# Kernel optimization log

Hardware: AMD Instinct MI355X
Metric: run time of the kernel (lower is better)

The kernel has to match this reference:

```python
import jax, jax.numpy as jnp
import numpy as np

N_DATA = 8192
M_QUERIES = 8192

def setup_inputs() -> dict:
    key = jax.random.key(0)
    k1, k2 = jax.random.split(key)
    data = jax.random.uniform(k1, (N_DATA, 3), dtype=jnp.float32)
    queries = jax.random.uniform(k2, (M_QUERIES, 3), dtype=jnp.float32)
    return {"data": data, "queries": queries, "radius": 0.1}

def reference(data, queries, radius):
    """Faithful jax version of native_neighbor_search.

    Returns (neighbors_index, neighbors_row_splits).
    Because jax.jit requires static shapes, neighbors_index is padded to the
    maximal size m*n with -1; the number of valid entries is
    neighbors_row_splits[-1]. Valid entries appear in the same row-major
    (query-ordered) order as torch's nonzero().
    """
    n = data.shape[0]
    m = queries.shape[0]
    # pairwise Euclidean distances [m, n] via the ||q||^2 + ||d||^2 - 2 q.d expansion
    q2 = jnp.sum(queries * queries, axis=1, keepdims=True)          # [m,1]
    d2 = jnp.sum(data * data, axis=1, keepdims=True).T              # [1,n]
    dists = jnp.sqrt(jnp.maximum(q2 + d2 - 2.0 * (queries @ data.T), 0.0))
    mask = dists <= radius                                          # [m,n]
    # CSR row splits: exclusive prefix sum of per-query neighbor counts
    counts = jnp.sum(mask.astype(jnp.int32), axis=1)                # [m]
    row_splits = jnp.concatenate(
        [jnp.zeros((1,), jnp.int32), jnp.cumsum(counts)])           # [m+1]
    # flattened nonzero in row-major order -> column index = flat % n
    (flat_idx,) = jnp.nonzero(mask.ravel(), size=m * n, fill_value=-1)
    neighbors_index = jnp.where(flat_idx >= 0, flat_idx % n, -1).astype(jnp.int32)
    return neighbors_index, row_splits
```

## Files before the change

### kernel.cpp

```cpp
#include <hip/hip_runtime.h>
#include <stdint.h>


#define N8 8192
#define C0 2097152

__device__ __forceinline__ float next_up(float x) {
    return __uint_as_float(__float_as_uint(x) + 1u);
}
__device__ __forceinline__ float next_down(float x) {
    return __uint_as_float(__float_as_uint(x) - 1u);
}

__device__ __forceinline__ float sq_threshold(float r) {
    float T = __fmul_rn(r, r);
    while (__fsqrt_rn(T) > r) T = next_down(T);
    while (__fsqrt_rn(next_up(T)) <= r) T = next_up(T);
    return T;
}

__device__ __forceinline__ float pair_metric(float qx, float qy, float qz, float q2,
                                             float dx, float dy, float dz) {
    float d2 = __fadd_rn(__fadd_rn(__fmul_rn(dx, dx), __fmul_rn(dy, dy)),
                         __fmul_rn(dz, dz));
    float dot = __builtin_fmaf(qz, dz, __builtin_fmaf(qy, dy, __fmul_rn(qx, dx)));
    return __fsub_rn(__fadd_rn(q2, d2), __fmul_rn(2.0f, dot));
}

__device__ __forceinline__ float bc_lane(float x, int j) {
    return __int_as_float(__builtin_amdgcn_readlane(__float_as_int(x), j));
}


__global__ __launch_bounds__(256) void count_then_fill(
    const float* __restrict__ data, const float* __restrict__ queries,
    const float* __restrict__ radius_p, int* __restrict__ out_idx,
    unsigned long long* __restrict__ masks, int* __restrict__ counts) {
    int bid = blockIdx.x;
    int lane = threadIdx.x & 63;
    int wv = threadIdx.x >> 6;

    {
        int u = bid * 4 + wv;
        int c = u >> 6;
        int g = u & 63;
        float T = sq_threshold(radius_p[0]);
        int p = c * 64 + lane;
        float dx = data[3 * p + 0], dy = data[3 * p + 1], dz = data[3 * p + 2];
        float d2 = __fadd_rn(__fadd_rn(__fmul_rn(dx, dx), __fmul_rn(dy, dy)),
                             __fmul_rn(dz, dz));
        for (int s = 0; s < 2; ++s) {
            int qbase = g * 128 + s * 64;
            int q = qbase + lane;
            float qx = queries[3 * q + 0], qy = queries[3 * q + 1],
                  qz = queries[3 * q + 2];
            float q2 = __fadd_rn(__fadd_rn(__fmul_rn(qx, qx), __fmul_rn(qy, qy)),
                                 __fmul_rn(qz, qz));
            unsigned long long parked = 0;
#pragma unroll
            for (int j = 0; j < 64; ++j) {
                float Qx = bc_lane(qx, j), Qy = bc_lane(qy, j);
                float Qz = bc_lane(qz, j), Q2 = bc_lane(q2, j);
                float dot = __builtin_fmaf(Qz, dz,
                              __builtin_fmaf(Qy, dy, __fmul_rn(Qx, dx)));
                float uu = __fsub_rn(__fadd_rn(Q2, d2), __fmul_rn(2.0f, dot));
                unsigned long long mk = __ballot(uu <= T);
                if (lane == j) parked = mk;
            }
            masks[(size_t)(qbase + lane) * 128 + c] = parked;
            atomicAdd(&counts[qbase + lane], __popcll(parked));
        }
    }

    int4* out4 = (int4*)out_idx;
    const int4 v = make_int4(-1, -1, -1, -1);
    const size_t n4 = (size_t)N8 * N8 / 4;
    size_t i = (size_t)(C0 / 4) + (size_t)bid * 256 + threadIdx.x;
    const size_t stride = 2048ull * 256ull;
    for (; i < n4; i += stride) out4[i] = v;
}

__global__ __launch_bounds__(1024) void scan_kernel2(const int* __restrict__ counts,
                                                     int* __restrict__ rs, int m) {
    __shared__ int part[1024];
    int t = threadIdx.x;
    int base = t * 8;
    int c[8];
    int s = 0;
    for (int k = 0; k < 8; ++k) {
        int p = base + k;
        c[k] = (p < m) ? counts[p] : 0;
        s += c[k];
    }
    part[t] = s;
    __syncthreads();
    for (int off = 1; off < 1024; off <<= 1) {
        int v = 0;
        if (t >= off) v = part[t - off];
        __syncthreads();
        if (t >= off) part[t] += v;
        __syncthreads();
    }
    int run = (t == 0) ? 0 : part[t - 1];
    for (int k = 0; k < 8; ++k) {
        int p = base + k;
        if (p < m) rs[p] = run;
        run += c[k];
    }
    if (t == 1023) rs[m] = part[1023];
}

__global__ __launch_bounds__(256) void emit_fill_tail(
    const unsigned long long* __restrict__ masks, const int* __restrict__ rs,
    int* __restrict__ out_idx) {
    int wave = threadIdx.x >> 6;
    int lane = threadIdx.x & 63;
    int q = blockIdx.x * 4 + wave;

    unsigned long long lo = masks[(size_t)q * 128 + lane];
    unsigned long long hi = masks[(size_t)q * 128 + 64 + lane];
    int plo = __popcll(lo), phi = __popcll(hi);
    int ilo = plo, ihi = phi;
    for (int off = 1; off < 64; off <<= 1) {
        int a = __shfl_up(ilo, off, 64);
        int b = __shfl_up(ihi, off, 64);
        if (lane >= off) { ilo += a; ihi += b; }
    }
    int total_lo = __shfl(ilo, 63, 64);
    int base = rs[q];
    int pos_lo = base + ilo - plo;
    int pos_hi = base + total_lo + ihi - phi;
    int jb_lo = lane * 64, jb_hi = (64 + lane) * 64;
    while (lo) {
        int b = __builtin_ctzll(lo);
        out_idx[pos_lo++] = jb_lo + b;
        lo &= lo - 1;
    }
    while (hi) {
        int b = __builtin_ctzll(hi);
        out_idx[pos_hi++] = jb_hi + b;
        hi &= hi - 1;
    }

    int L = rs[N8];
    int Lr = (L + 3) & ~3;
    if (blockIdx.x == 0 && (int)threadIdx.x < (Lr - L))
        out_idx[L + threadIdx.x] = -1;
    int4* out4 = (int4*)out_idx;
    const int4 v = make_int4(-1, -1, -1, -1);
    const int c04 = C0 >> 2;
    int i = (Lr >> 2) + blockIdx.x * 256 + threadIdx.x;
    const int stride = 2048 * 256;
    for (; i < c04; i += stride) out4[i] = v;
}


__global__ __launch_bounds__(256) void fill_kernel(int* __restrict__ out, size_t total) {
    size_t n4 = total >> 2;
    int4* out4 = (int4*)out;
    size_t i = (size_t)blockIdx.x * blockDim.x + threadIdx.x;
    size_t stride = (size_t)gridDim.x * blockDim.x;
    const int4 v = make_int4(-1, -1, -1, -1);
    for (; i < n4; i += stride) out4[i] = v;
    if (blockIdx.x == 0 && threadIdx.x == 0) {
        for (size_t k = n4 << 2; k < total; ++k) out[k] = -1;
    }
}

__global__ __launch_bounds__(256) void count_kernel(
    const float* __restrict__ data, const float* __restrict__ queries,
    const float* __restrict__ radius_p, int n, int m, int* __restrict__ counts) {
    int q = (blockIdx.x * blockDim.x + threadIdx.x) >> 6;
    int lane = threadIdx.x & 63;
    if (q >= m) return;
    float r = radius_p[0];
    float T = sq_threshold(r);
    float qx = queries[3 * q + 0], qy = queries[3 * q + 1], qz = queries[3 * q + 2];
    float q2 = __fadd_rn(__fadd_rn(__fmul_rn(qx, qx), __fmul_rn(qy, qy)),
                         __fmul_rn(qz, qz));
    int cnt = 0;
    for (int j = lane; j < n; j += 64) {
        float u = pair_metric(qx, qy, qz, q2, data[3 * j], data[3 * j + 1], data[3 * j + 2]);
        if (u <= T) cnt++;
    }
    for (int off = 32; off > 0; off >>= 1) cnt += __shfl_down(cnt, off, 64);
    if (lane == 0) counts[q] = cnt;
}

__global__ __launch_bounds__(256) void emit_kernel(
    const float* __restrict__ data, const float* __restrict__ queries,
    const float* __restrict__ radius_p, int n, int m,
    const int* __restrict__ row_splits, int* __restrict__ out_idx) {
    int q = (blockIdx.x * blockDim.x + threadIdx.x) >> 6;
    int lane = threadIdx.x & 63;
    if (q >= m) return;
    float r = radius_p[0];
    float T = sq_threshold(r);
    float qx = queries[3 * q + 0], qy = queries[3 * q + 1], qz = queries[3 * q + 2];
    float q2 = __fadd_rn(__fadd_rn(__fmul_rn(qx, qx), __fmul_rn(qy, qy)),
                         __fmul_rn(qz, qz));
    int base = row_splits[q];
    unsigned long long lane_mask_lt = (lane == 0) ? 0ULL : (~0ULL >> (64 - lane));
    for (int j0 = 0; j0 < n; j0 += 64) {
        int j = j0 + lane;
        bool pred = false;
        if (j < n) {
            float u = pair_metric(qx, qy, qz, q2, data[3 * j], data[3 * j + 1], data[3 * j + 2]);
            pred = (u <= T);
        }
        unsigned long long mask = __ballot(pred);
        if (pred) {
            int pos = base + __popcll(mask & lane_mask_lt);
            out_idx[pos] = j;
        }
        base += __popcll(mask);
    }
}


extern "C" void kernel_launch(void* const* d_in, const int* in_sizes, int n_in,
                              void* d_out, int out_size, void* d_ws, size_t ws_size,
                              hipStream_t stream) {
    const float* data = (const float*)d_in[0];
    const float* queries = (const float*)d_in[1];
    const float* radius = (const float*)d_in[2];
    int n = in_sizes[0] / 3;
    int m = in_sizes[1] / 3;
    int* out = (int*)d_out;
    size_t idx_count = (size_t)m * (size_t)n;
    int* row = out + idx_count;

    size_t mask_bytes = (size_t)N8 * 128 * 8;
    size_t need = mask_bytes + N8 * 4;
    bool fast = (n == N8) && (m == N8) && (ws_size >= need);

    if (fast) {
        unsigned long long* masks = (unsigned long long*)d_ws;
        int* counts = (int*)((char*)d_ws + mask_bytes);
        hipMemsetAsync(counts, 0, N8 * sizeof(int), stream);
        count_then_fill<<<2048, 256, 0, stream>>>(data, queries, radius, out,
                                                  masks, counts);
        scan_kernel2<<<1, 1024, 0, stream>>>(counts, row, m);
        emit_fill_tail<<<2048, 256, 0, stream>>>(masks, row, out);
    } else {
        fill_kernel<<<2048, 256, 0, stream>>>(out, idx_count);
        int blocks = (m * 64 + 255) / 256;
        count_kernel<<<blocks, 256, 0, stream>>>(data, queries, radius, n, m, row);
        scan_kernel2<<<1, 1024, 0, stream>>>(row, row, m);
        emit_kernel<<<blocks, 256, 0, stream>>>(data, queries, radius, n, m, row, out);
    }
}
```

Baseline: 77.53 us.

## Fuse prefix scan into emit kernel with redundant per-block scan

```diff
diff --git a/kernel.cpp b/kernel.cpp
--- a/kernel.cpp
+++ b/kernel.cpp
@@ -4,6 +4,8 @@
 
 #define N8 8192
 #define C0 2097152
+#define C04 (C0 / 4)
+#define N4TOT ((size_t)N8 * N8 / 4)
 
 __device__ __forceinline__ float next_up(float x) {
     return __uint_as_float(__float_as_uint(x) + 1u);
@@ -31,127 +33,132 @@
     return __int_as_float(__builtin_amdgcn_readlane(__float_as_int(x), j));
 }
 
+__device__ __forceinline__ void count_unit(
+    int u, const float* __restrict__ data, const float* __restrict__ queries,
+    float T, unsigned long long* __restrict__ masks, int* __restrict__ counts) {
+    int lane = threadIdx.x & 63;
+    int c = u >> 6;
+    int g = u & 63;
+    int p = c * 64 + lane;
+    float dx = data[3 * p + 0], dy = data[3 * p + 1], dz = data[3 * p + 2];
+    float d2 = __fadd_rn(__fadd_rn(__fmul_rn(dx, dx), __fmul_rn(dy, dy)),
+                         __fmul_rn(dz, dz));
+    for (int s = 0; s < 2; ++s) {
+        int qbase = g * 128 + s * 64;
+        int q = qbase + lane;
+        float qx = queries[3 * q + 0], qy = queries[3 * q + 1],
+              qz = queries[3 * q + 2];
+        float q2 = __fadd_rn(__fadd_rn(__fmul_rn(qx, qx), __fmul_rn(qy, qy)),
+                             __fmul_rn(qz, qz));
+        unsigned long long parked = 0;
+#pragma unroll
+        for (int j = 0; j < 64; ++j) {
+            float Qx = bc_lane(qx, j), Qy = bc_lane(qy, j);
+            float Qz = bc_lane(qz, j), Q2 = bc_lane(q2, j);
+            float dot = __builtin_fmaf(Qz, dz,
+                          __builtin_fmaf(Qy, dy, __fmul_rn(Qx, dx)));
+            float uu = __fsub_rn(__fadd_rn(Q2, d2), __fmul_rn(2.0f, dot));
+            unsigned long long mk = __ballot(uu <= T);
+            if (lane == j) parked = mk;
+        }
+        masks[(size_t)(qbase + lane) * 128 + c] = parked;
+        atomicAdd(&counts[qbase + lane], __popcll(parked));
+    }
+}
+
 
 __global__ __launch_bounds__(256) void count_then_fill(
     const float* __restrict__ data, const float* __restrict__ queries,
     const float* __restrict__ radius_p, int* __restrict__ out_idx,
     unsigned long long* __restrict__ masks, int* __restrict__ counts) {
     int bid = blockIdx.x;
-    int lane = threadIdx.x & 63;
     int wv = threadIdx.x >> 6;
-
     {
-        int u = bid * 4 + wv;
-        int c = u >> 6;
-        int g = u & 63;
         float T = sq_threshold(radius_p[0]);
-        int p = c * 64 + lane;
-        float dx = data[3 * p + 0], dy = data[3 * p + 1], dz = data[3 * p + 2];
-        float d2 = __fadd_rn(__fadd_rn(__fmul_rn(dx, dx), __fmul_rn(dy, dy)),
-                             __fmul_rn(dz, dz));
-        for (int s = 0; s < 2; ++s) {
-            int qbase = g * 128 + s * 64;
-            int q = qbase + lane;
-            float qx = queries[3 * q + 0], qy = queries[3 * q + 1],
-                  qz = queries[3 * q + 2];
-            float q2 = __fadd_rn(__fadd_rn(__fmul_rn(qx, qx), __fmul_rn(qy, qy)),
-                                 __fmul_rn(qz, qz));
-            unsigned long long parked = 0;
-#pragma unroll
-            for (int j = 0; j < 64; ++j) {
-                float Qx = bc_lane(qx, j), Qy = bc_lane(qy, j);
-                float Qz = bc_lane(qz, j), Q2 = bc_lane(q2, j);
-                float dot = __builtin_fmaf(Qz, dz,
-                              __builtin_fmaf(Qy, dy, __fmul_rn(Qx, dx)));
-                float uu = __fsub_rn(__fadd_rn(Q2, d2), __fmul_rn(2.0f, dot));
-                unsigned long long mk = __ballot(uu <= T);
-                if (lane == j) parked = mk;
-            }
-            masks[(size_t)(qbase + lane) * 128 + c] = parked;
-            atomicAdd(&counts[qbase + lane], __popcll(parked));
-        }
-    }
-
+        count_unit(bid * 4 + wv, data, queries, T, masks, counts);
+    }
     int4* out4 = (int4*)out_idx;
     const int4 v = make_int4(-1, -1, -1, -1);
-    const size_t n4 = (size_t)N8 * N8 / 4;
-    size_t i = (size_t)(C0 / 4) + (size_t)bid * 256 + threadIdx.x;
+    size_t i = (size_t)C04 + (size_t)bid * 256 + threadIdx.x;
     const size_t stride = 2048ull * 256ull;
-    for (; i < n4; i += stride) out4[i] = v;
-}
-
-__global__ __launch_bounds__(1024) void scan_kernel2(const int* __restrict__ counts,
-                                                     int* __restrict__ rs, int m) {
-    __shared__ int part[1024];
+    for (; i < N4TOT; i += stride) out4[i] = v;
+}
+
+__global__ __launch_bounds__(256) void scanemit_fill_tail(
+    const unsigned long long* __restrict__ masks, const int* __restrict__ counts,
+    int* __restrict__ out_idx, int* __restrict__ rs) {
+    __shared__ int part[256];
+    __shared__ int s_cnt[32];
+    __shared__ int s_base[4];
+    int b = blockIdx.x;
     int t = threadIdx.x;
-    int base = t * 8;
-    int c[8];
+    int wave = t >> 6;
+    int lane = t & 63;
+
     int s = 0;
-    for (int k = 0; k < 8; ++k) {
-        int p = base + k;
-        c[k] = (p < m) ? counts[p] : 0;
-        s += c[k];
-    }
+#pragma unroll 8
+    for (int k = 0; k < 32; ++k) s += counts[t * 32 + k];
     part[t] = s;
     __syncthreads();
-    for (int off = 1; off < 1024; off <<= 1) {
+    for (int off = 1; off < 256; off <<= 1) {
         int v = 0;
         if (t >= off) v = part[t - off];
         __syncthreads();
         if (t >= off) part[t] += v;
         __syncthreads();
     }
-    int run = (t == 0) ? 0 : part[t - 1];
-    for (int k = 0; k < 8; ++k) {
-        int p = base + k;
-        if (p < m) rs[p] = run;
-        run += c[k];
-    }
-    if (t == 1023) rs[m] = part[1023];
-}
-
-__global__ __launch_bounds__(256) void emit_fill_tail(
-    const unsigned long long* __restrict__ masks, const int* __restrict__ rs,
-    int* __restrict__ out_idx) {
-    int wave = threadIdx.x >> 6;
-    int lane = threadIdx.x & 63;
-    int q = blockIdx.x * 4 + wave;
-
-    unsigned long long lo = masks[(size_t)q * 128 + lane];
-    unsigned long long hi = masks[(size_t)q * 128 + 64 + lane];
-    int plo = __popcll(lo), phi = __popcll(hi);
-    int ilo = plo, ihi = phi;
-    for (int off = 1; off < 64; off <<= 1) {
-        int a = __shfl_up(ilo, off, 64);
-        int b = __shfl_up(ihi, off, 64);
-        if (lane >= off) { ilo += a; ihi += b; }
-    }
-    int total_lo = __shfl(ilo, 63, 64);
-    int base = rs[q];
-    int pos_lo = base + ilo - plo;
-    int pos_hi = base + total_lo + ihi - phi;
-    int jb_lo = lane * 64, jb_hi = (64 + lane) * 64;
-    while (lo) {
-        int b = __builtin_ctzll(lo);
-        out_idx[pos_lo++] = jb_lo + b;
-        lo &= lo - 1;
-    }
-    while (hi) {
-        int b = __builtin_ctzll(hi);
-        out_idx[pos_hi++] = jb_hi + b;
-        hi &= hi - 1;
-    }
-
-    int L = rs[N8];
+    int c32 = b >> 3;
+    if (t < 32) s_cnt[t] = counts[c32 * 32 + t];
+    __syncthreads();
+    if (t < 4) {
+        int q = b * 4 + t;
+        int excl = (c32 == 0) ? 0 : part[c32 - 1];
+        int o = q & 31;
+        int sum = 0;
+        for (int k = 0; k < o; ++k) sum += s_cnt[k];
+        int v = excl + sum;
+        s_base[t] = v;
+        rs[q] = v;
+    }
+    if (b == 2047 && t == 0) rs[N8] = part[255];
+    __syncthreads();
+    int L = part[255];
+
+    {
+        int q = b * 4 + wave;
+        unsigned long long lo = masks[(size_t)q * 128 + lane];
+        unsigned long long hi = masks[(size_t)q * 128 + 64 + lane];
+        int plo = __popcll(lo), phi = __popcll(hi);
+        int ilo = plo, ihi = phi;
+        for (int off = 1; off < 64; off <<= 1) {
+            int a = __shfl_up(ilo, off, 64);
+            int bsh = __shfl_up(ihi, off, 64);
+            if (lane >= off) { ilo += a; ihi += bsh; }
+        }
+        int total_lo = __shfl(ilo, 63, 64);
+        int base = s_base[wave];
+        int pos_lo = base + ilo - plo;
+        int pos_hi = base + total_lo + ihi - phi;
+        int jb_lo = lane * 64, jb_hi = (64 + lane) * 64;
+        while (lo) {
+            int bt = __builtin_ctzll(lo);
+            out_idx[pos_lo++] = jb_lo + bt;
+            lo &= lo - 1;
+        }
+        while (hi) {
+            int bt = __builtin_ctzll(hi);
+            out_idx[pos_hi++] = jb_hi + bt;
+            hi &= hi - 1;
+        }
+    }
+
     int Lr = (L + 3) & ~3;
-    if (blockIdx.x == 0 && (int)threadIdx.x < (Lr - L))
-        out_idx[L + threadIdx.x] = -1;
+    if (b == 0 && t < (Lr - L)) out_idx[L + t] = -1;
     int4* out4 = (int4*)out_idx;
     const int4 v = make_int4(-1, -1, -1, -1);
-    const int c04 = C0 >> 2;
-    int i = (Lr >> 2) + blockIdx.x * 256 + threadIdx.x;
+    int i = (Lr >> 2) + b * 256 + t;
     const int stride = 2048 * 256;
-    for (; i < c04; i += stride) out4[i] = v;
+    for (; i < C04; i += stride) out4[i] = v;
 }
 
 
@@ -185,6 +192,36 @@
     }
     for (int off = 32; off > 0; off >>= 1) cnt += __shfl_down(cnt, off, 64);
     if (lane == 0) counts[q] = cnt;
+}
+
+__global__ __launch_bounds__(1024) void scan_kernel2(const int* __restrict__ counts,
+                                                     int* __restrict__ rs, int m) {
+    __shared__ int part[1024];
+    int t = threadIdx.x;
+    int base = t * 8;
+    int c[8];
+    int s = 0;
+    for (int k = 0; k < 8; ++k) {
+        int p = base + k;
+        c[k] = (p < m) ? counts[p] : 0;
+        s += c[k];
+    }
+    part[t] = s;
+    __syncthreads();
+    for (int off = 1; off < 1024; off <<= 1) {
+        int v = 0;
+        if (t >= off) v = part[t - off];
+        __syncthreads();
+        if (t >= off) part[t] += v;
+        __syncthreads();
+    }
+    int run = (t == 0) ? 0 : part[t - 1];
+    for (int k = 0; k < 8; ++k) {
+        int p = base + k;
+        if (p < m) rs[p] = run;
+        run += c[k];
+    }
+    if (t == 1023) rs[m] = part[1023];
 }
 
 __global__ __launch_bounds__(256) void emit_kernel(
@@ -240,8 +277,7 @@
         hipMemsetAsync(counts, 0, N8 * sizeof(int), stream);
         count_then_fill<<<2048, 256, 0, stream>>>(data, queries, radius, out,
                                                   masks, counts);
-        scan_kernel2<<<1, 1024, 0, stream>>>(counts, row, m);
-        emit_fill_tail<<<2048, 256, 0, stream>>>(masks, row, out);
+        scanemit_fill_tail<<<2048, 256, 0, stream>>>(masks, counts, out, row);
     } else {
         fill_kernel<<<2048, 256, 0, stream>>>(out, idx_count);
         int blocks = (m * 64 + 255) / 256;
```

Measured after the change: 75.40 us. 2.7% less time.
